# Kernel optimization log

Hardware: AMD Instinct MI355X
Metric: run time of the kernel (lower is better)

Reference implementation:

```python
import jax, jax.numpy as jnp
import numpy as np

N_NODE = 100000
EMB = 128
N_EDGES = 1600000
LAYERS = 2
EPS = 1e-12  # torch F.normalize default eps


def setup_inputs() -> dict:
    key = jax.random.key(0)
    k1, k2, k3, k4, k5, k6 = jax.random.split(key, 6)
    return {
        "user_emb_weight": jax.random.normal(k1, (N_NODE, EMB), jnp.float32) * 0.02,
        "gate_w": jax.random.normal(k2, (EMB, EMB), jnp.float32) * (1.0 / np.sqrt(EMB)),
        "gate_b": jax.random.normal(k3, (EMB,), jnp.float32) * 0.01,
        "edge_rows": jax.random.randint(k4, (N_EDGES,), 0, N_NODE, jnp.int32),
        "edge_cols": jax.random.randint(k5, (N_EDGES,), 0, N_NODE, jnp.int32),
        "edge_vals": jax.random.uniform(k6, (N_EDGES,), jnp.float32),
        "layers": LAYERS,
    }


def _spmm(rows, cols, vals, x, n):
    # sparse [n,n] @ dense [n,d]: out[r] += v * x[c]
    gathered = vals[:, None] * x[cols]          # [nnz, d]
    return jax.ops.segment_sum(gathered, rows, num_segments=n)


def _l2_normalize(x):
    norm = jnp.sqrt(jnp.sum(x * x, axis=1, keepdims=True))
    return x / jnp.maximum(norm, EPS)


def reference(user_emb_weight, gate_w, gate_b, edge_rows, edge_cols, edge_vals, layers):
    n = user_emb_weight.shape[0]
    # self_gating: em * sigmoid(em @ W + b)
    u = user_emb_weight * jax.nn.sigmoid(user_emb_weight @ gate_w + gate_b)
    acc = u
    for _ in range(layers):
        u = _spmm(edge_rows, edge_cols, edge_vals, u, n)
        acc = acc + _l2_normalize(u)
    return acc
```

## Files before the change

### kernel.cpp

```cpp
#include <hip/hip_runtime.h>


typedef short s16x8 __attribute__((ext_vector_type(8)));
typedef float f32x4 __attribute__((ext_vector_type(4)));

__device__ __forceinline__ float bflo(unsigned u) {
    union { unsigned u; float f; } x; x.u = u << 16; return x.f;
}
__device__ __forceinline__ float bfhi(unsigned u) {
    union { unsigned u; float f; } x; x.u = u & 0xffff0000u; return x.f;
}
__device__ __forceinline__ float bf1(unsigned short s) {
    union { unsigned u; float f; } x; x.u = (unsigned)s << 16; return x.f;
}
__device__ __forceinline__ unsigned short f2bf(float f) {
    union { float f; unsigned u; } x; x.f = f;
    unsigned r = x.u + 0x7fffu + ((x.u >> 16) & 1u);
    return (unsigned short)(r >> 16);
}
__device__ __forceinline__ unsigned pack2(float a, float b) {
    return (unsigned)f2bf(a) | ((unsigned)f2bf(b) << 16);
}
__device__ __forceinline__ float i2f(int i) {
    union { int i; float f; } x; x.i = i; return x.f;
}
__device__ __forceinline__ int f2i(float f) {
    union { float f; int i; } x; x.f = f; return x.i;
}

__global__ void detect_kernel(const unsigned* __restrict__ em, int nwords,
                              int* __restrict__ mode) {
    __shared__ int bad_s;
    if (threadIdx.x == 0) bad_s = 0;
    __syncthreads();
    int bad = 0;
    for (int i = threadIdx.x; i < nwords; i += blockDim.x) {
        unsigned u = em[i];
        unsigned e0 = (u >> 7) & 0xFFu;
        unsigned e1 = (u >> 23) & 0xFFu;
        if (e0 >= 157u || e1 >= 157u) bad = 1;
    }
    if (bad) atomicOr(&bad_s, 1);
    __syncthreads();
    if (threadIdx.x == 0) mode[0] = bad_s;
}

__global__ __launch_bounds__(256) void gating_mfma_kernel(
    const void* __restrict__ emv, const void* __restrict__ Wv,
    const void* __restrict__ bv,
    unsigned short* __restrict__ u_out, void* __restrict__ acc_out,
    const int* __restrict__ mode_p, int n)
{
    __shared__ __align__(16) unsigned short Wt[128 * 136];
    const int fp32 = mode_p[0];
    const int tid = threadIdx.x;

    if (fp32) {
        const float* W = (const float*)Wv;
        for (int i = tid; i < 16384; i += 256) {
            int k = i >> 7, c = i & 127;
            Wt[c * 136 + k] = f2bf(W[i]);
        }
    } else {
        const unsigned short* W = (const unsigned short*)Wv;
        for (int i = tid; i < 16384; i += 256) {
            int k = i >> 7, c = i & 127;
            Wt[c * 136 + k] = W[i];
        }
    }
    __syncthreads();

    const int wave = tid >> 6, lane = tid & 63;
    const int quad = lane >> 4, l16 = lane & 15;

    s16x8 bfrag[8][4];
#pragma unroll
    for (int t = 0; t < 8; ++t)
#pragma unroll
        for (int kb = 0; kb < 4; ++kb) {
            int col = t * 16 + l16;
            int k = kb * 32 + quad * 8;
            bfrag[t][kb] = *(const s16x8*)&Wt[col * 136 + k];
        }

    float bias[8];
    if (fp32) {
        const float* b = (const float*)bv;
#pragma unroll
        for (int t = 0; t < 8; ++t) bias[t] = b[t * 16 + l16];
    } else {
        const unsigned short* b = (const unsigned short*)bv;
#pragma unroll
        for (int t = 0; t < 8; ++t) bias[t] = bf1(b[t * 16 + l16]);
    }

    const int nstrips = (n + 15) >> 4;
    const int gwaves = gridDim.x * 4;
    for (int s = blockIdx.x * 4 + wave; s < nstrips; s += gwaves) {
        const int m0 = s * 16;
        const int arow = m0 + l16;

        s16x8 afrag[4];
        if (fp32) {
            const float* em = (const float*)emv;
#pragma unroll
            for (int kb = 0; kb < 4; ++kb) {
                union { unsigned u[4]; s16x8 v; } cv;
                if (arow < n) {
                    const float* src = em + (size_t)arow * 128 + kb * 32 + quad * 8;
                    float4 f0 = *(const float4*)(src);
                    float4 f1 = *(const float4*)(src + 4);
                    cv.u[0] = pack2(f0.x, f0.y); cv.u[1] = pack2(f0.z, f0.w);
                    cv.u[2] = pack2(f1.x, f1.y); cv.u[3] = pack2(f1.z, f1.w);
                } else { cv.u[0] = cv.u[1] = cv.u[2] = cv.u[3] = 0; }
                afrag[kb] = cv.v;
            }
        } else {
            const unsigned short* em = (const unsigned short*)emv;
#pragma unroll
            for (int kb = 0; kb < 4; ++kb) {
                union { uint4 u; s16x8 v; } cv;
                if (arow < n)
                    cv.u = *(const uint4*)(em + (size_t)arow * 128 + kb * 32 + quad * 8);
                else
                    cv.u = make_uint4(0, 0, 0, 0);
                afrag[kb] = cv.v;
            }
        }

        f32x4 acc[8];
#pragma unroll
        for (int t = 0; t < 8; ++t) {
            f32x4 a = {0.f, 0.f, 0.f, 0.f};
#pragma unroll
            for (int kb = 0; kb < 4; ++kb)
                a = __builtin_amdgcn_mfma_f32_16x16x32_bf16(afrag[kb], bfrag[t][kb], a, 0, 0, 0);
            acc[t] = a;
        }

#pragma unroll
        for (int t = 0; t < 8; ++t) {
            const int col = t * 16 + l16;
#pragma unroll
            for (int r = 0; r < 4; ++r) {
                const int row = m0 + quad * 4 + r;
                if (row < n) {
                    float e;
                    if (fp32) e = ((const float*)emv)[(size_t)row * 128 + col];
                    else      e = bf1(((const unsigned short*)emv)[(size_t)row * 128 + col]);
                    float g = 1.f / (1.f + __expf(-(acc[t][r] + bias[t])));
                    float o = e * g;
                    unsigned short ob = f2bf(o);
                    u_out[(size_t)row * 128 + col] = ob;
                    if (fp32) ((float*)acc_out)[(size_t)row * 128 + col] = o;
                    else      ((unsigned short*)acc_out)[(size_t)row * 128 + col] = ob;
                }
            }
        }
    }
}

#define CHUNK 4096
#define MAXE  5120

__global__ __launch_bounds__(256) void bucket_hist_kernel(
    const int* __restrict__ erow, int* __restrict__ bcnt, int nnz)
{
    __shared__ int l[512];
    int tid = threadIdx.x;
    l[tid] = 0; l[tid + 256] = 0;
    __syncthreads();
    int c0 = blockIdx.x * CHUNK;
    int cend = min(c0 + CHUNK, nnz);
    for (int i = c0 + tid; i < cend; i += 256)
        atomicAdd(&l[(unsigned)erow[i] >> 8], 1);
    __syncthreads();
    if (l[tid]) atomicAdd(&bcnt[tid], l[tid]);
    if (l[tid + 256]) atomicAdd(&bcnt[tid + 256], l[tid + 256]);
}

__global__ __launch_bounds__(256) void bucket_scan_kernel(
    const int* __restrict__ bcnt, int* __restrict__ bbase,
    int* __restrict__ gcursor, int* __restrict__ rp, int n, int B, int nnz)
{
    __shared__ int s[512], tsum[256];
    int tid = threadIdx.x;
    s[tid] = (tid < B) ? bcnt[tid] : 0;
    s[tid + 256] = (tid + 256 < B) ? bcnt[tid + 256] : 0;
    __syncthreads();
    int a0 = s[2 * tid], a1 = s[2 * tid + 1];
    tsum[tid] = a0 + a1;
    __syncthreads();
#pragma unroll
    for (int off = 1; off < 256; off <<= 1) {
        int t = (tid >= off) ? tsum[tid - off] : 0;
        __syncthreads();
        tsum[tid] += t;
        __syncthreads();
    }
    int excl = (tid == 0) ? 0 : tsum[tid - 1];
    if (2 * tid < B)     { bbase[2 * tid] = excl;          gcursor[2 * tid] = excl; }
    if (2 * tid + 1 < B) { bbase[2 * tid + 1] = excl + a0; gcursor[2 * tid + 1] = excl + a0; }
    if (tid == 0) { bbase[B] = nnz; rp[n] = nnz; }
}

__global__ __launch_bounds__(256) void partition_kernel(
    const int* __restrict__ erow, const int* __restrict__ ecol,
    const void* __restrict__ eval, int* __restrict__ gcursor,
    int2* __restrict__ sev_tmp, const int* __restrict__ mode_p, int nnz)
{
    __shared__ int lcnt[512], lbase[512];
    int tid = threadIdx.x;
    lcnt[tid] = 0; lcnt[tid + 256] = 0;
    __syncthreads();
    int c0 = blockIdx.x * CHUNK;
    int cend = min(c0 + CHUNK, nnz);
    for (int i = c0 + tid; i < cend; i += 256)
        atomicAdd(&lcnt[(unsigned)erow[i] >> 8], 1);
    __syncthreads();
    int c256 = lcnt[tid], c512 = lcnt[tid + 256];
    if (c256 > 0) lbase[tid] = atomicAdd(&gcursor[tid], c256);
    if (c512 > 0) lbase[tid + 256] = atomicAdd(&gcursor[tid + 256], c512);
    __syncthreads();
    lcnt[tid] = 0; lcnt[tid + 256] = 0;
    __syncthreads();
    const int fp32 = mode_p[0];
    for (int i = c0 + tid; i < cend; i += 256) {
        int row = erow[i];
        int bkt = (unsigned)row >> 8;
        int rank = atomicAdd(&lcnt[bkt], 1);
        float v = fp32 ? ((const float*)eval)[i]
                       : bf1(((const unsigned short*)eval)[i]);
        int x = ((row & 255) << 17) | ecol[i];
        sev_tmp[lbase[bkt] + rank] = make_int2(x, f2i(v));
    }
}

__global__ __launch_bounds__(256) void csr_fin_kernel(
    const int* __restrict__ bbase, const int2* __restrict__ sev_tmp,
    int2* __restrict__ sev, int* __restrict__ rp, int n)
{
    __shared__ int2 ev[MAXE];
    __shared__ int rcnt[256], tsum[256];
    int b = blockIdx.x;
    int base = bbase[b];
    int size = bbase[b + 1] - base;
    int tid = threadIdx.x;
    rcnt[tid] = 0;
    __syncthreads();
    bool fits = (size <= MAXE);
    if (fits) {
        for (int e = tid; e < size; e += 256) {
            int2 t = sev_tmp[base + e];
            ev[e] = t;
            atomicAdd(&rcnt[(unsigned)t.x >> 17], 1);
        }
    } else {
        for (int e = tid; e < size; e += 256)
            atomicAdd(&rcnt[(unsigned)sev_tmp[base + e].x >> 17], 1);
    }
    __syncthreads();
    int myc = rcnt[tid];
    tsum[tid] = myc;
    __syncthreads();
#pragma unroll
    for (int off = 1; off < 256; off <<= 1) {
        int t = (tid >= off) ? tsum[tid - off] : 0;
        __syncthreads();
        tsum[tid] += t;
        __syncthreads();
    }
    int excl = tsum[tid] - myc;
    int row0 = b << 8;
    if (row0 + tid < n) rp[row0 + tid] = base + excl;
    __syncthreads();
    rcnt[tid] = excl;
    __syncthreads();
    for (int e = tid; e < size; e += 256) {
        int2 t = fits ? ev[e] : sev_tmp[base + e];
        int r = (unsigned)t.x >> 17;
        int k = atomicAdd(&rcnt[r], 1);
        sev[base + k] = make_int2(t.x & 0x1FFFF, t.y);
    }
}

__global__ __launch_bounds__(256) void spmm_norm_kernel(
    const int* __restrict__ rp, const int2* __restrict__ sev,
    const uint4* __restrict__ u_in, uint4* __restrict__ u_out,
    void* __restrict__ acc, const int* __restrict__ mode_p, int n)
{
    int w = (int)((blockIdx.x * (unsigned)blockDim.x + threadIdx.x) >> 6);
    int lane = threadIdx.x & 63;
    if (w >= n) return;
    const int q = lane >> 4, l16 = lane & 15;
    int e0 = rp[w], e1 = rp[w + 1];
    float a[8] = {0, 0, 0, 0, 0, 0, 0, 0};

    if (e1 > e0) {
        int e = e0;
        for (; e + 8 <= e1; e += 8) {
            int2 m0 = sev[e + q];
            int2 m1 = sev[e + 4 + q];
            uint4 g0 = u_in[(size_t)m0.x * 16 + l16];
            uint4 g1 = u_in[(size_t)m1.x * 16 + l16];
            float v0 = i2f(m0.y), v1 = i2f(m1.y);
            a[0] = fmaf(v0, bflo(g0.x), a[0]); a[1] = fmaf(v0, bfhi(g0.x), a[1]);
            a[2] = fmaf(v0, bflo(g0.y), a[2]); a[3] = fmaf(v0, bfhi(g0.y), a[3]);
            a[4] = fmaf(v0, bflo(g0.z), a[4]); a[5] = fmaf(v0, bfhi(g0.z), a[5]);
            a[6] = fmaf(v0, bflo(g0.w), a[6]); a[7] = fmaf(v0, bfhi(g0.w), a[7]);
            a[0] = fmaf(v1, bflo(g1.x), a[0]); a[1] = fmaf(v1, bfhi(g1.x), a[1]);
            a[2] = fmaf(v1, bflo(g1.y), a[2]); a[3] = fmaf(v1, bfhi(g1.y), a[3]);
            a[4] = fmaf(v1, bflo(g1.z), a[4]); a[5] = fmaf(v1, bfhi(g1.z), a[5]);
            a[6] = fmaf(v1, bflo(g1.w), a[6]); a[7] = fmaf(v1, bfhi(g1.w), a[7]);
        }
        for (; e < e1; e += 4) {
            int idx = e + q;
            int safe = min(idx, e1 - 1);
            int2 m = sev[safe];
            float v = (idx < e1) ? i2f(m.y) : 0.f;
            uint4 g = u_in[(size_t)m.x * 16 + l16];
            a[0] = fmaf(v, bflo(g.x), a[0]); a[1] = fmaf(v, bfhi(g.x), a[1]);
            a[2] = fmaf(v, bflo(g.y), a[2]); a[3] = fmaf(v, bfhi(g.y), a[3]);
            a[4] = fmaf(v, bflo(g.z), a[4]); a[5] = fmaf(v, bfhi(g.z), a[5]);
            a[6] = fmaf(v, bflo(g.w), a[6]); a[7] = fmaf(v, bfhi(g.w), a[7]);
        }
    }

#pragma unroll
    for (int j = 0; j < 8; ++j) {
        a[j] += __shfl_xor(a[j], 16, 64);
        a[j] += __shfl_xor(a[j], 32, 64);
    }
    float s = 0.f;
#pragma unroll
    for (int j = 0; j < 8; ++j) s = fmaf(a[j], a[j], s);
#pragma unroll
    for (int off = 8; off > 0; off >>= 1) s += __shfl_xor(s, off, 64);
    float scale = 1.f / fmaxf(sqrtf(s), 1e-12f);

    if (q == 0 && u_out) {
        uint4 o;
        o.x = pack2(a[0], a[1]); o.y = pack2(a[2], a[3]);
        o.z = pack2(a[4], a[5]); o.w = pack2(a[6], a[7]);
        u_out[(size_t)w * 16 + l16] = o;
    }
    if (q == 1) {
        if (mode_p[0]) {
            float* ap = (float*)acc + (size_t)w * 128 + l16 * 8;
            float4 c0 = *(float4*)ap, c1 = *(float4*)(ap + 4);
            c0.x += a[0] * scale; c0.y += a[1] * scale;
            c0.z += a[2] * scale; c0.w += a[3] * scale;
            c1.x += a[4] * scale; c1.y += a[5] * scale;
            c1.z += a[6] * scale; c1.w += a[7] * scale;
            *(float4*)ap = c0; *(float4*)(ap + 4) = c1;
        } else {
            uint4* ap = (uint4*)acc + (size_t)w * 16 + l16;
            uint4 c = *ap;
            c.x = pack2(bflo(c.x) + a[0] * scale, bfhi(c.x) + a[1] * scale);
            c.y = pack2(bflo(c.y) + a[2] * scale, bfhi(c.y) + a[3] * scale);
            c.z = pack2(bflo(c.z) + a[4] * scale, bfhi(c.z) + a[5] * scale);
            c.w = pack2(bflo(c.w) + a[6] * scale, bfhi(c.w) + a[7] * scale);
            *ap = c;
        }
    }
}

extern "C" void kernel_launch(void* const* d_in, const int* in_sizes, int n_in,
                              void* d_out, int out_size, void* d_ws, size_t ws_size,
                              hipStream_t stream)
{
    const void* em   = d_in[0];
    const void* gw   = d_in[1];
    const void* gb   = d_in[2];
    const int*  erow = (const int*)d_in[3];
    const int*  ecol = (const int*)d_in[4];
    const void* eval = d_in[5];

    int n   = in_sizes[0] / 128;
    int nnz = in_sizes[3];
    int B   = (n + 255) >> 8;
    int nblk_e = (nnz + CHUNK - 1) / CHUNK;

    char* ws = (char*)d_ws;
    size_t off = 0;
    auto carve = [&](size_t bytes) -> void* {
        void* p = ws + off;
        off += (bytes + 255) & ~(size_t)255;
        return p;
    };
    size_t nd = (size_t)n * 128;
    int*      mode    = (int*)carve(4);
    unsigned* uA      = (unsigned*)carve(nd * 2);
    unsigned* uB      = (unsigned*)carve(nd * 2);
    int*      rp      = (int*)carve((size_t)(n + 1) * 4);
    int*      bcnt    = (int*)carve(512 * 4);
    int*      bbase   = (int*)carve(516 * 4);
    int*      gcursor = (int*)carve(512 * 4);
    int2*     sev     = (int2*)carve((size_t)nnz * 8);
    int2*     sev_tmp = (int2*)uB;

    hipMemsetAsync(bcnt, 0, 512 * 4, stream);
    detect_kernel<<<1, 256, 0, stream>>>((const unsigned*)em, 8192, mode);

    gating_mfma_kernel<<<512, 256, 0, stream>>>(em, gw, gb, (unsigned short*)uA, d_out, mode, n);
    bucket_hist_kernel<<<nblk_e, 256, 0, stream>>>(erow, bcnt, nnz);
    bucket_scan_kernel<<<1, 256, 0, stream>>>(bcnt, bbase, gcursor, rp, n, B, nnz);
    partition_kernel<<<nblk_e, 256, 0, stream>>>(erow, ecol, eval, gcursor, sev_tmp, mode, nnz);
    csr_fin_kernel<<<B, 256, 0, stream>>>(bbase, sev_tmp, sev, rp, n);

    spmm_norm_kernel<<<(n + 3) / 4, 256, 0, stream>>>(
        rp, sev, (const uint4*)uA, (uint4*)uB, d_out, mode, n);
    spmm_norm_kernel<<<(n + 3) / 4, 256, 0, stream>>>(
        rp, sev, (const uint4*)uB, (uint4*)nullptr, d_out, mode, n);
}
```

Baseline: 387.9 us.

## Defer accumulator writes to final SpMM pass using stored per-row norm scales

The gating kernel no longer writes the gated embedding into the output, and the first SpMM pass no longer does a read-modify-write of the output. The first pass now stores only a per-row normalization scale. The second pass builds the final result in one write, from the bf16 gated embedding, the bf16 layer-1 embedding times its saved scale, and its own normalized result. This cuts the repeated full-size output traffic, which is fp32 in fp32 mode, down to one write plus two bf16 reads. In exchange, in fp32 mode the output now uses bf16-rounded copies of the gated and layer-1 terms instead of fp32 values, which slightly loosens accuracy.

```diff
diff --git a/kernel.cpp b/kernel.cpp
--- a/kernel.cpp
+++ b/kernel.cpp
@@ -48,7 +48,7 @@
 __global__ __launch_bounds__(256) void gating_mfma_kernel(
     const void* __restrict__ emv, const void* __restrict__ Wv,
     const void* __restrict__ bv,
-    unsigned short* __restrict__ u_out, void* __restrict__ acc_out,
+    unsigned short* __restrict__ u_out,
     const int* __restrict__ mode_p, int n)
 {
     __shared__ __align__(16) unsigned short Wt[128 * 136];
@@ -149,11 +149,7 @@
                     if (fp32) e = ((const float*)emv)[(size_t)row * 128 + col];
                     else      e = bf1(((const unsigned short*)emv)[(size_t)row * 128 + col]);
                     float g = 1.f / (1.f + __expf(-(acc[t][r] + bias[t])));
-                    float o = e * g;
-                    unsigned short ob = f2bf(o);
-                    u_out[(size_t)row * 128 + col] = ob;
-                    if (fp32) ((float*)acc_out)[(size_t)row * 128 + col] = o;
-                    else      ((unsigned short*)acc_out)[(size_t)row * 128 + col] = ob;
+                    u_out[(size_t)row * 128 + col] = f2bf(e * g);
                 }
             }
         }
@@ -287,7 +283,10 @@
 __global__ __launch_bounds__(256) void spmm_norm_kernel(
     const int* __restrict__ rp, const int2* __restrict__ sev,
     const uint4* __restrict__ u_in, uint4* __restrict__ u_out,
-    void* __restrict__ acc, const int* __restrict__ mode_p, int n)
+    float* __restrict__ scale_out,
+    const uint4* __restrict__ g_in, const uint4* __restrict__ prev_u,
+    const float* __restrict__ prev_scale,
+    void* __restrict__ out, const int* __restrict__ mode_p, int n)
 {
     int w = (int)((blockIdx.x * (unsigned)blockDim.x + threadIdx.x) >> 6);
     int lane = threadIdx.x & 63;
@@ -344,23 +343,31 @@
         o.z = pack2(a[4], a[5]); o.w = pack2(a[6], a[7]);
         u_out[(size_t)w * 16 + l16] = o;
     }
-    if (q == 1) {
+    if (lane == 0 && scale_out) scale_out[w] = scale;
+
+    if (q == 1 && prev_u) {
+        float s1 = prev_scale[w];
+        uint4 gv = g_in[(size_t)w * 16 + l16];
+        uint4 p1 = prev_u[(size_t)w * 16 + l16];
+        float r0 = bflo(gv.x) + bflo(p1.x) * s1 + a[0] * scale;
+        float r1 = bfhi(gv.x) + bfhi(p1.x) * s1 + a[1] * scale;
+        float r2 = bflo(gv.y) + bflo(p1.y) * s1 + a[2] * scale;
+        float r3 = bfhi(gv.y) + bfhi(p1.y) * s1 + a[3] * scale;
+        float r4 = bflo(gv.z) + bflo(p1.z) * s1 + a[4] * scale;
+        float r5 = bfhi(gv.z) + bfhi(p1.z) * s1 + a[5] * scale;
+        float r6 = bflo(gv.w) + bflo(p1.w) * s1 + a[6] * scale;
+        float r7 = bfhi(gv.w) + bfhi(p1.w) * s1 + a[7] * scale;
         if (mode_p[0]) {
-            float* ap = (float*)acc + (size_t)w * 128 + l16 * 8;
-            float4 c0 = *(float4*)ap, c1 = *(float4*)(ap + 4);
-            c0.x += a[0] * scale; c0.y += a[1] * scale;
-            c0.z += a[2] * scale; c0.w += a[3] * scale;
-            c1.x += a[4] * scale; c1.y += a[5] * scale;
-            c1.z += a[6] * scale; c1.w += a[7] * scale;
+            float* ap = (float*)out + (size_t)w * 128 + l16 * 8;
+            float4 c0, c1;
+            c0.x = r0; c0.y = r1; c0.z = r2; c0.w = r3;
+            c1.x = r4; c1.y = r5; c1.z = r6; c1.w = r7;
             *(float4*)ap = c0; *(float4*)(ap + 4) = c1;
         } else {
-            uint4* ap = (uint4*)acc + (size_t)w * 16 + l16;
-            uint4 c = *ap;
-            c.x = pack2(bflo(c.x) + a[0] * scale, bfhi(c.x) + a[1] * scale);
-            c.y = pack2(bflo(c.y) + a[2] * scale, bfhi(c.y) + a[3] * scale);
-            c.z = pack2(bflo(c.z) + a[4] * scale, bfhi(c.z) + a[5] * scale);
-            c.w = pack2(bflo(c.w) + a[6] * scale, bfhi(c.w) + a[7] * scale);
-            *ap = c;
+            uint4 o;
+            o.x = pack2(r0, r1); o.y = pack2(r2, r3);
+            o.z = pack2(r4, r5); o.w = pack2(r6, r7);
+            ((uint4*)out)[(size_t)w * 16 + l16] = o;
         }
     }
 }
@@ -393,6 +400,7 @@
     unsigned* uA      = (unsigned*)carve(nd * 2);
     unsigned* uB      = (unsigned*)carve(nd * 2);
     int*      rp      = (int*)carve((size_t)(n + 1) * 4);
+    float*    scale1  = (float*)carve((size_t)n * 4);
     int*      bcnt    = (int*)carve(512 * 4);
     int*      bbase   = (int*)carve(516 * 4);
     int*      gcursor = (int*)carve(512 * 4);
@@ -402,14 +410,16 @@
     hipMemsetAsync(bcnt, 0, 512 * 4, stream);
     detect_kernel<<<1, 256, 0, stream>>>((const unsigned*)em, 8192, mode);
 
-    gating_mfma_kernel<<<512, 256, 0, stream>>>(em, gw, gb, (unsigned short*)uA, d_out, mode, n);
+    gating_mfma_kernel<<<512, 256, 0, stream>>>(em, gw, gb, (unsigned short*)uA, mode, n);
     bucket_hist_kernel<<<nblk_e, 256, 0, stream>>>(erow, bcnt, nnz);
     bucket_scan_kernel<<<1, 256, 0, stream>>>(bcnt, bbase, gcursor, rp, n, B, nnz);
     partition_kernel<<<nblk_e, 256, 0, stream>>>(erow, ecol, eval, gcursor, sev_tmp, mode, nnz);
     csr_fin_kernel<<<B, 256, 0, stream>>>(bbase, sev_tmp, sev, rp, n);
 
     spmm_norm_kernel<<<(n + 3) / 4, 256, 0, stream>>>(
-        rp, sev, (const uint4*)uA, (uint4*)uB, d_out, mode, n);
+        rp, sev, (const uint4*)uA, (uint4*)uB, scale1,
+        nullptr, nullptr, nullptr, nullptr, mode, n);
     spmm_norm_kernel<<<(n + 3) / 4, 256, 0, stream>>>(
-        rp, sev, (const uint4*)uB, (uint4*)nullptr, d_out, mode, n);
-}
+        rp, sev, (const uint4*)uB, nullptr, nullptr,
+        (const uint4*)uA, (const uint4*)uB, scale1, d_out, mode, n);
+}
```

Result: faster. 363.7 us (-6.2%).
